# Optimization experiments

Measured on AMD Instinct MI355X. Metric: run time of the kernel, lower is better.

Reference implementation:

```python
import jax, jax.numpy as jnp
import numpy as np

A = 256      # alphabet_size
T = 128      # tag_vector_dim
E = 64       # embedding_dim
H = 64       # hidden_dim (encoder)
NL = 3       # num_layers
B = 4096     # batch
L = 32       # lemma length
STEPS = 30   # decode steps
START = 1    # Alphabet.start_integer (external global in source; fixed here)


def _cell(x, h, c, Wih, Whh, bih, bhh):
    # torch LSTM gate order: i, f, g, o
    g = x @ Wih.T + h @ Whh.T + bih + bhh
    i, f, gg, o = jnp.split(g, 4, axis=-1)
    c = jax.nn.sigmoid(f) * c + jax.nn.sigmoid(i) * jnp.tanh(gg)
    h = jax.nn.sigmoid(o) * jnp.tanh(c)
    return h, c


def _run_layer(xs, Wih, Whh, bih, bhh):
    # xs: [L, B, D] -> ys: [L, B, Hout]; zero initial state (torch default)
    Hout = Whh.shape[1]
    h0 = jnp.zeros((xs.shape[1], Hout), xs.dtype)
    def step(carry, x):
        h, c = _cell(x, carry[0], carry[1], Wih, Whh, bih, bhh)
        return (h, c), h
    _, ys = jax.lax.scan(step, (h0, h0), xs)
    return ys


def setup_inputs() -> dict:
    key = jax.random.key(0)
    ks = jax.random.split(key, 24)
    s = 0.05
    inp = {
        'families': jax.random.randint(ks[0], (B,), 0, 10),
        'languages': jax.random.randint(ks[1], (B,), 0, 20),
        'tags': jax.random.uniform(ks[2], (B, T), dtype=jnp.float32),
        'lemmata': jax.random.randint(ks[3], (B, L), 0, A),
        'emb': jax.random.normal(ks[4], (A, E), jnp.float32) * s,
        # encoder lstm1: layer0 in=T+E, layers 1..2 in=H; hidden=H
        'l1_Wih0': jax.random.normal(ks[5], (4 * H, T + E), jnp.float32) * s,
        'l1_Whh0': jax.random.normal(ks[6], (4 * H, H), jnp.float32) * s,
        'l1_bih0': jnp.zeros((4 * H,), jnp.float32),
        'l1_bhh0': jnp.zeros((4 * H,), jnp.float32),
        'l1_Wih': jax.random.normal(ks[7], (NL - 1, 4 * H, H), jnp.float32) * s,
        'l1_Whh': jax.random.normal(ks[8], (NL - 1, 4 * H, H), jnp.float32) * s,
        'l1_bih': jnp.zeros((NL - 1, 4 * H), jnp.float32),
        'l1_bhh': jnp.zeros((NL - 1, 4 * H), jnp.float32),
        # decoder lstm2: layer0 in=T+A, layers 1..2 in=A; hidden=A
        'l2_Wih0': jax.random.normal(ks[9], (4 * A, T + A), jnp.float32) * s,
        'l2_Whh0': jax.random.normal(ks[10], (4 * A, A), jnp.float32) * s,
        'l2_bih0': jnp.zeros((4 * A,), jnp.float32),
        'l2_bhh0': jnp.zeros((4 * A,), jnp.float32),
        'l2_Wih': jax.random.normal(ks[11], (NL - 1, 4 * A, A), jnp.float32) * s,
        'l2_Whh': jax.random.normal(ks[12], (NL - 1, 4 * A, A), jnp.float32) * s,
        'l2_bih': jnp.zeros((NL - 1, 4 * A), jnp.float32),
        'l2_bhh': jnp.zeros((NL - 1, 4 * A), jnp.float32),
        'lin_W': jax.random.normal(ks[13], (A, A), jnp.float32) * s,
        'lin_b': jnp.zeros((A,), jnp.float32),
    }
    return inp


def reference(families, languages, tags, lemmata, emb,
              l1_Wih0, l1_Whh0, l1_bih0, l1_bhh0, l1_Wih, l1_Whh, l1_bih, l1_bhh,
              l2_Wih0, l2_Whh0, l2_bih0, l2_bhh0, l2_Wih, l2_Whh, l2_bih, l2_bhh,
              lin_W, lin_b):
    tags = tags.astype(jnp.float32)
    # ---- encoder (computed as in source; its output is discarded there too) ----
    x = emb[lemmata]                                   # [B, L, E]
    tags_rep = jnp.broadcast_to(tags[:, None, :], (B, L, T))
    enc_in = jnp.concatenate([x, tags_rep], axis=-1)   # [B, L, E+T]
    ys = jnp.swapaxes(enc_in, 0, 1)                    # [L, B, E+T]
    ys = _run_layer(ys, l1_Wih0, l1_Whh0, l1_bih0, l1_bhh0)
    for k in range(NL - 1):
        ys = _run_layer(ys, l1_Wih[k], l1_Whh[k], l1_bih[k], l1_bhh[k])
    code = ys  # unused downstream, matching original (hidden/cell reset to zero)

    start = jax.nn.one_hot(jnp.full((B,), START), A, dtype=jnp.float32)  # [B, A]
    h0 = jnp.zeros((NL, B, A), jnp.float32)
    c0 = jnp.zeros((NL, B, A), jnp.float32)

    def dstep(carry, _):
        prob, h, c = carry
        xin = jnp.concatenate([prob, tags], axis=-1)   # [B, A+T]
        h0_, c0_ = _cell(xin, h[0], c[0], l2_Wih0, l2_Whh0, l2_bih0, l2_bhh0)
        h1_, c1_ = _cell(h0_, h[1], c[1], l2_Wih[0], l2_Whh[0], l2_bih[0], l2_bhh[0])
        h2_, c2_ = _cell(h1_, h[2], c[2], l2_Wih[1], l2_Whh[1], l2_bih[1], l2_bhh[1])
        pred = jax.nn.sigmoid(h2_ @ lin_W.T + lin_b)   # [B, A]
        new_carry = (pred, jnp.stack([h0_, h1_, h2_]), jnp.stack([c0_, c1_, c2_]))
        return new_carry, (pred, jnp.argmax(pred, axis=-1))

    _, (preds, outs) = jax.lax.scan(dstep, (start, h0, c0), None, length=STEPS)
    probabilities = jnp.concatenate(
        [start[:, None, :], jnp.swapaxes(preds, 0, 1)], axis=1)  # [B, 31, A]
    outputs = jnp.swapaxes(outs, 0, 1)                           # [B, 30]
    return probabilities, outputs
```

## Files before the change

kernel.cpp:

```cpp
#include <hip/hip_runtime.h>
#include <math.h>


typedef float v4 __attribute__((ext_vector_type(4)));

constexpr int Bsz   = 4096;
constexpr int AA    = 256;
constexpr int STEPS = 30;
constexpr int LDP   = 31 * AA;
constexpr long long PROB_N = (long long)Bsz * 31 * AA;

constexpr int WP0_Q = 160 * 1024;
constexpr int WP1_Q = 128 * 1024;
constexpr int WP2_Q = 128 * 1024;
constexpr int WPL_Q = 64 * 256;
constexpr int WP1_BASE = WP0_Q;
constexpr int WP2_BASE = WP1_BASE + WP1_Q;
constexpr int WPL_BASE = WP2_BASE + WP2_Q;
constexpr int WP_TOTAL = WPL_BASE + WPL_Q;

constexpr int XROWS = 1152;

__device__ __forceinline__ float sigf(float x) { return 1.0f / (1.0f + expf(-x)); }

__global__ void repack_kernel(const float* __restrict__ Wih0, const float* __restrict__ Whh0,
                              const float* __restrict__ Wih12, const float* __restrict__ Whh12,
                              const float* __restrict__ linW, float* __restrict__ ws)
{
    int t = blockIdx.x * 256 + threadIdx.x;
    v4 val;
    if (t < WP1_BASE) {
        int cg = t & 15, j = (t >> 4) & 3, c = (t >> 6) & 15, q = t >> 10;
        int grow = j * 256 + c * 16 + cg;
        int k4 = q * 4;
        const float* src = (k4 < 384) ? (Wih0 + grow * 384 + k4)
                                      : (Whh0 + grow * 256 + (k4 - 384));
        val = *reinterpret_cast<const v4*>(src);
    } else if (t < WP2_BASE) {
        int tt = t - WP1_BASE;
        int cg = tt & 15, j = (tt >> 4) & 3, c = (tt >> 6) & 15, q = tt >> 10;
        int grow = j * 256 + c * 16 + cg;
        int k4 = q * 4;
        const float* src = (k4 < 256) ? (Wih12 + grow * 256 + k4)
                                      : (Whh12 + grow * 256 + (k4 - 256));
        val = *reinterpret_cast<const v4*>(src);
    } else if (t < WPL_BASE) {
        int tt = t - WP2_BASE;
        int cg = tt & 15, j = (tt >> 4) & 3, c = (tt >> 6) & 15, q = tt >> 10;
        int grow = j * 256 + c * 16 + cg;
        int k4 = q * 4;
        const float* src = (k4 < 256) ? (Wih12 + 262144 + grow * 256 + k4)
                                      : (Whh12 + 262144 + grow * 256 + (k4 - 256));
        val = *reinterpret_cast<const v4*>(src);
    } else {
        int tt = t - WPL_BASE;
        int cg = tt & 15, c = (tt >> 4) & 15, q = tt >> 8;
        int n = c * 16 + cg;
        val = *reinterpret_cast<const v4*>(linW + n * 256 + q * 4);
    }
    reinterpret_cast<v4*>(ws)[t] = val;
}

#define FMA_BLOCK(W, Xv)                                   \
    _Pragma("unroll")                                      \
    for (int k = 0; k < 4; k++)                            \
        _Pragma("unroll")                                  \
        for (int j = 0; j < 4; j++)                        \
            _Pragma("unroll")                              \
            for (int r = 0; r < 4; r++)                    \
                acc[j][r] += W[j][k] * Xv[k][r];

template<int Q>
__device__ __forceinline__ void lstm_phase(
    const v4* __restrict__ wq, const float* __restrict__ xb,
    const float* __restrict__ bihL, const float* __restrict__ bhhL,
    int u, int rg, float (&cr)[4], float* __restrict__ dst)
{
    float bs[4];
    #pragma unroll
    for (int j = 0; j < 4; j++) bs[j] = bihL[j * 256 + u] + bhhL[j * 256 + u];

    float acc[4][4];
    #pragma unroll
    for (int j = 0; j < 4; j++)
        #pragma unroll
        for (int r = 0; r < 4; r++) acc[j][r] = 0.0f;

    const v4* xq = reinterpret_cast<const v4*>(xb) + rg;
    const v4* wp = wq;
    v4 wa[4], wb[4], xa[4], xc[4];

    #pragma unroll
    for (int j = 0; j < 4; j++) wa[j] = wp[j * 16];
    wp += 1024;
    #pragma unroll
    for (int k = 0; k < 4; k++) xa[k] = xq[k * 4];

    #pragma unroll 1
    for (int q = 0; q < Q - 2; q += 2) {
        #pragma unroll
        for (int j = 0; j < 4; j++) wb[j] = wp[j * 16];
        wp += 1024;
        #pragma unroll
        for (int k = 0; k < 4; k++) xc[k] = xq[(q + 1) * 16 + k * 4];
        FMA_BLOCK(wa, xa)
        #pragma unroll
        for (int j = 0; j < 4; j++) wa[j] = wp[j * 16];
        wp += 1024;
        #pragma unroll
        for (int k = 0; k < 4; k++) xa[k] = xq[(q + 2) * 16 + k * 4];
        FMA_BLOCK(wb, xc)
    }
    #pragma unroll
    for (int j = 0; j < 4; j++) wb[j] = wp[j * 16];
    #pragma unroll
    for (int k = 0; k < 4; k++) xc[k] = xq[(Q - 1) * 16 + k * 4];
    FMA_BLOCK(wa, xa)
    FMA_BLOCK(wb, xc)

    __syncthreads();
    v4 hv;
    #pragma unroll
    for (int r = 0; r < 4; r++) {
        float gi = acc[0][r] + bs[0];
        float gf = acc[1][r] + bs[1];
        float gg = acc[2][r] + bs[2];
        float go = acc[3][r] + bs[3];
        float cn = sigf(gf) * cr[r] + sigf(gi) * tanhf(gg);
        cr[r] = cn;
        hv[r] = sigf(go) * tanhf(cn);
    }
    *reinterpret_cast<v4*>(dst + u * 16 + rg * 4) = hv;
    __syncthreads();
}

__device__ __forceinline__ void lin_phase(
    const v4* __restrict__ wq, const float* __restrict__ xb,
    const float* __restrict__ linb,
    int n, int rg, int m0, int t,
    float* __restrict__ probdst, float* __restrict__ out)
{
    float b = linb[n];
    float acc[4] = {0.f, 0.f, 0.f, 0.f};
    const v4* xq = reinterpret_cast<const v4*>(xb) + rg;
    const v4* wp = wq;
    v4 wa, wb, xa[4], xc[4];

    wa = wp[0]; wp += 256;
    #pragma unroll
    for (int k = 0; k < 4; k++) xa[k] = xq[k * 4];

    #pragma unroll 1
    for (int q = 0; q < 62; q += 2) {
        wb = wp[0]; wp += 256;
        #pragma unroll
        for (int k = 0; k < 4; k++) xc[k] = xq[(q + 1) * 16 + k * 4];
        #pragma unroll
        for (int k = 0; k < 4; k++)
            #pragma unroll
            for (int r = 0; r < 4; r++) acc[r] += wa[k] * xa[k][r];
        wa = wp[0]; wp += 256;
        #pragma unroll
        for (int k = 0; k < 4; k++) xa[k] = xq[(q + 2) * 16 + k * 4];
        #pragma unroll
        for (int k = 0; k < 4; k++)
            #pragma unroll
            for (int r = 0; r < 4; r++) acc[r] += wb[k] * xc[k][r];
    }
    wb = wp[0];
    #pragma unroll
    for (int k = 0; k < 4; k++) xc[k] = xq[63 * 16 + k * 4];
    #pragma unroll
    for (int k = 0; k < 4; k++)
        #pragma unroll
        for (int r = 0; r < 4; r++) acc[r] += wa[k] * xa[k][r];
    #pragma unroll
    for (int k = 0; k < 4; k++)
        #pragma unroll
        for (int r = 0; r < 4; r++) acc[r] += wb[k] * xc[k][r];

    __syncthreads();
    v4 pv;
    #pragma unroll
    for (int r = 0; r < 4; r++) pv[r] = sigf(acc[r] + b);
    *reinterpret_cast<v4*>(probdst + n * 16 + rg * 4) = pv;
    #pragma unroll
    for (int r = 0; r < 4; r++)
        out[(long long)(m0 + rg * 4 + r) * LDP + (long long)(t + 1) * AA + n] = pv[r];
    __syncthreads();
}

__global__ __launch_bounds__(1024, 4) void decode_kernel(
    const float* __restrict__ tags,
    const float* __restrict__ bih0, const float* __restrict__ bhh0,
    const float* __restrict__ bih12, const float* __restrict__ bhh12,
    const float* __restrict__ linb,
    const float* __restrict__ ws,
    float* __restrict__ out)
{
    __shared__ float X[XROWS * 16];
    __shared__ float redv[1024];
    __shared__ int   redi[1024];

    const int tid  = threadIdx.x;
    const int c    = tid >> 6;
    const int lane = tid & 63;
    const int cg   = lane & 15;
    const int rg   = lane >> 4;
    const int u    = c * 16 + cg;
    const int m0   = blockIdx.x * 16;

    for (int i = tid; i < XROWS * 16; i += 1024) X[i] = 0.0f;
    __syncthreads();
    for (int i = tid; i < 128 * 16; i += 1024) {
        int m = i & 15, k = i >> 4;
        X[(256 + k) * 16 + m] = tags[(long long)(m0 + m) * 128 + k];
    }
    if (tid < 16) X[1 * 16 + tid] = 1.0f;
    for (int i = tid; i < 256 * 16; i += 1024) {
        int m = i >> 8, col = i & 255;
        out[(long long)(m0 + m) * LDP + col] = (col == 1) ? 1.0f : 0.0f;
    }
    __syncthreads();

    float cr0[4], cr1[4], cr2[4];
    #pragma unroll
    for (int r = 0; r < 4; r++) { cr0[r] = 0.f; cr1[r] = 0.f; cr2[r] = 0.f; }

    const v4* wsq = reinterpret_cast<const v4*>(ws);
    const v4* w0 = wsq + 0        + c * 64 + cg;
    const v4* w1 = wsq + WP1_BASE + c * 64 + cg;
    const v4* w2 = wsq + WP2_BASE + c * 64 + cg;
    const v4* wl = wsq + WPL_BASE + c * 16 + cg;

    float* hx0 = X + 384 * 16;
    float* hx1 = X + 640 * 16;
    float* hx2 = X + 896 * 16;

    const int arow = tid & 15, sb = tid >> 4;
    float* outputs = out + PROB_N;

    #pragma unroll 1
    for (int t = 0; t < STEPS; t++) {
        lstm_phase<160>(w0, X,   bih0,         bhh0,         u, rg, cr0, hx0);
        lstm_phase<128>(w1, hx0, bih12,        bhh12,        u, rg, cr1, hx1);
        lstm_phase<128>(w2, hx1, bih12 + 1024, bhh12 + 1024, u, rg, cr2, hx2);
        lin_phase(wl, hx2, linb, u, rg, m0, t, X, out);

        float bv = -1.0f; int bi = 0;
        #pragma unroll
        for (int i = 0; i < 4; i++) {
            int uu = sb * 4 + i;
            float v = X[uu * 16 + arow];
            if (v > bv) { bv = v; bi = uu; }
        }
        redv[sb * 16 + arow] = bv;
        redi[sb * 16 + arow] = bi;
        __syncthreads();
        if (tid < 16) {
            float v0 = redv[tid]; int i0 = redi[tid];
            #pragma unroll 1
            for (int s = 1; s < 64; s++) {
                float v = redv[s * 16 + tid]; int ii = redi[s * 16 + tid];
                if (v > v0 || (v == v0 && ii < i0)) { v0 = v; i0 = ii; }
            }
            outputs[(long long)(m0 + tid) * STEPS + t] = (float)i0;
        }
    }
}

extern "C" void kernel_launch(void* const* d_in, const int* in_sizes, int n_in,
                              void* d_out, int out_size, void* d_ws, size_t ws_size,
                              hipStream_t stream) {
    const float* tags  = (const float*)d_in[2];
    const float* Wih0  = (const float*)d_in[13];
    const float* Whh0  = (const float*)d_in[14];
    const float* bih0  = (const float*)d_in[15];
    const float* bhh0  = (const float*)d_in[16];
    const float* Wih12 = (const float*)d_in[17];
    const float* Whh12 = (const float*)d_in[18];
    const float* bih12 = (const float*)d_in[19];
    const float* bhh12 = (const float*)d_in[20];
    const float* linW  = (const float*)d_in[21];
    const float* linb  = (const float*)d_in[22];

    float* out = (float*)d_out;
    float* ws  = (float*)d_ws;

    repack_kernel<<<WP_TOTAL / 256, 256, 0, stream>>>(Wih0, Whh0, Wih12, Whh12,
                                                      linW, ws);
    decode_kernel<<<Bsz / 16, 1024, 0, stream>>>(
        tags, bih0, bhh0, bih12, bhh12, linb, ws, out);
}
```

Measured before the change: 7.847 ms.

## Stream decoder weights into an LDS ring via async global-to-LDS loads

```diff
diff --git a/kernel.cpp b/kernel.cpp
--- a/kernel.cpp
+++ b/kernel.cpp
@@ -22,6 +22,15 @@
 constexpr int XROWS = 1152;
 
 __device__ __forceinline__ float sigf(float x) { return 1.0f / (1.0f + expf(-x)); }
+
+__device__ __forceinline__ void gld16(const float* g, float* l) {
+    __builtin_amdgcn_global_load_lds(
+        (const __attribute__((address_space(1))) float*)g,
+        (__attribute__((address_space(3))) float*)l,
+        16, 0, 0);
+}
+
+#define WAITVM(n) asm volatile("s_waitcnt vmcnt(" #n ")" ::: "memory")
 
 __global__ void repack_kernel(const float* __restrict__ Wih0, const float* __restrict__ Whh0,
                               const float* __restrict__ Wih12, const float* __restrict__ Whh12,
@@ -61,20 +70,38 @@
     reinterpret_cast<v4*>(ws)[t] = val;
 }
 
-#define FMA_BLOCK(W, Xv)                                   \
-    _Pragma("unroll")                                      \
-    for (int k = 0; k < 4; k++)                            \
-        _Pragma("unroll")                                  \
-        for (int j = 0; j < 4; j++)                        \
-            _Pragma("unroll")                              \
-            for (int r = 0; r < 4; r++)                    \
-                acc[j][r] += W[j][k] * Xv[k][r];
+#define LSTM_CHUNK(q)                                                          \
+    {                                                                          \
+        const v4* wv_ = (const v4*)(wbuf + (((q) & 3) << 12)) + cg;            \
+        v4 w_[4], x_[4];                                                       \
+        _Pragma("unroll") for (int j = 0; j < 4; j++) w_[j] = wv_[j * 16];     \
+        _Pragma("unroll") for (int k = 0; k < 4; k++) x_[k] = xq[(q) * 16 + k * 4]; \
+        _Pragma("unroll") for (int k = 0; k < 4; k++)                          \
+            _Pragma("unroll") for (int j = 0; j < 4; j++)                      \
+                _Pragma("unroll") for (int r = 0; r < 4; r++)                  \
+                    acc[j][r] += w_[j][k] * x_[k][r];                          \
+    }
+
+#define LIN_GROUP(g)                                                           \
+    {                                                                          \
+        const v4* wv_ = (const v4*)(wbuf + (((g) & 3) << 12)) + cg;            \
+        _Pragma("unroll") for (int s = 0; s < 4; s++) {                        \
+            v4 w_ = wv_[s * 16];                                               \
+            v4 x_[4];                                                          \
+            _Pragma("unroll") for (int k = 0; k < 4; k++)                      \
+                x_[k] = xq[((g) * 4 + s) * 16 + k * 4];                        \
+            _Pragma("unroll") for (int k = 0; k < 4; k++)                      \
+                _Pragma("unroll") for (int r = 0; r < 4; r++)                  \
+                    acc[r] += w_[k] * x_[k][r];                                \
+        }                                                                      \
+    }
 
 template<int Q>
-__device__ __forceinline__ void lstm_phase(
-    const v4* __restrict__ wq, const float* __restrict__ xb,
+__device__ __forceinline__ void lstm_phase_async(
+    const float* __restrict__ wg, float* __restrict__ wbuf,
+    const float* __restrict__ xb,
     const float* __restrict__ bihL, const float* __restrict__ bhhL,
-    int u, int rg, float (&cr)[4], float* __restrict__ dst)
+    int u, int rg, int cg, float (&cr)[4], float* __restrict__ dst)
 {
     float bs[4];
     #pragma unroll
@@ -87,36 +114,20 @@
         for (int r = 0; r < 4; r++) acc[j][r] = 0.0f;
 
     const v4* xq = reinterpret_cast<const v4*>(xb) + rg;
-    const v4* wp = wq;
-    v4 wa[4], wb[4], xa[4], xc[4];
-
-    #pragma unroll
-    for (int j = 0; j < 4; j++) wa[j] = wp[j * 16];
-    wp += 1024;
-    #pragma unroll
-    for (int k = 0; k < 4; k++) xa[k] = xq[k * 4];
+
+    gld16(wg,            wbuf);
+    gld16(wg +  1 * 4096, wbuf + 1 * 4096);
+    gld16(wg +  2 * 4096, wbuf + 2 * 4096);
 
     #pragma unroll 1
-    for (int q = 0; q < Q - 2; q += 2) {
-        #pragma unroll
-        for (int j = 0; j < 4; j++) wb[j] = wp[j * 16];
-        wp += 1024;
-        #pragma unroll
-        for (int k = 0; k < 4; k++) xc[k] = xq[(q + 1) * 16 + k * 4];
-        FMA_BLOCK(wa, xa)
-        #pragma unroll
-        for (int j = 0; j < 4; j++) wa[j] = wp[j * 16];
-        wp += 1024;
-        #pragma unroll
-        for (int k = 0; k < 4; k++) xa[k] = xq[(q + 2) * 16 + k * 4];
-        FMA_BLOCK(wb, xc)
-    }
-    #pragma unroll
-    for (int j = 0; j < 4; j++) wb[j] = wp[j * 16];
-    #pragma unroll
-    for (int k = 0; k < 4; k++) xc[k] = xq[(Q - 1) * 16 + k * 4];
-    FMA_BLOCK(wa, xa)
-    FMA_BLOCK(wb, xc)
+    for (int q = 0; q < Q - 3; q++) {
+        gld16(wg + (q + 3) * 4096, wbuf + (((q + 3) & 3) << 12));
+        WAITVM(3);
+        LSTM_CHUNK(q)
+    }
+    WAITVM(2); LSTM_CHUNK(Q - 3)
+    WAITVM(1); LSTM_CHUNK(Q - 2)
+    WAITVM(0); LSTM_CHUNK(Q - 1)
 
     __syncthreads();
     v4 hv;
@@ -134,50 +145,29 @@
     __syncthreads();
 }
 
-__device__ __forceinline__ void lin_phase(
-    const v4* __restrict__ wq, const float* __restrict__ xb,
-    const float* __restrict__ linb,
-    int n, int rg, int m0, int t,
+__device__ __forceinline__ void lin_phase_async(
+    const float* __restrict__ wg, float* __restrict__ wbuf,
+    const float* __restrict__ xb, const float* __restrict__ linb,
+    int n, int rg, int cg, int m0, int t,
     float* __restrict__ probdst, float* __restrict__ out)
 {
     float b = linb[n];
     float acc[4] = {0.f, 0.f, 0.f, 0.f};
     const v4* xq = reinterpret_cast<const v4*>(xb) + rg;
-    const v4* wp = wq;
-    v4 wa, wb, xa[4], xc[4];
-
-    wa = wp[0]; wp += 256;
-    #pragma unroll
-    for (int k = 0; k < 4; k++) xa[k] = xq[k * 4];
+
+    gld16(wg,            wbuf);
+    gld16(wg + 1 * 4096, wbuf + 1 * 4096);
+    gld16(wg + 2 * 4096, wbuf + 2 * 4096);
 
     #pragma unroll 1
-    for (int q = 0; q < 62; q += 2) {
-        wb = wp[0]; wp += 256;
-        #pragma unroll
-        for (int k = 0; k < 4; k++) xc[k] = xq[(q + 1) * 16 + k * 4];
-        #pragma unroll
-        for (int k = 0; k < 4; k++)
-            #pragma unroll
-            for (int r = 0; r < 4; r++) acc[r] += wa[k] * xa[k][r];
-        wa = wp[0]; wp += 256;
-        #pragma unroll
-        for (int k = 0; k < 4; k++) xa[k] = xq[(q + 2) * 16 + k * 4];
-        #pragma unroll
-        for (int k = 0; k < 4; k++)
-            #pragma unroll
-            for (int r = 0; r < 4; r++) acc[r] += wb[k] * xc[k][r];
-    }
-    wb = wp[0];
-    #pragma unroll
-    for (int k = 0; k < 4; k++) xc[k] = xq[63 * 16 + k * 4];
-    #pragma unroll
-    for (int k = 0; k < 4; k++)
-        #pragma unroll
-        for (int r = 0; r < 4; r++) acc[r] += wa[k] * xa[k][r];
-    #pragma unroll
-    for (int k = 0; k < 4; k++)
-        #pragma unroll
-        for (int r = 0; r < 4; r++) acc[r] += wb[k] * xc[k][r];
+    for (int g = 0; g < 13; g++) {
+        gld16(wg + (g + 3) * 4096, wbuf + (((g + 3) & 3) << 12));
+        WAITVM(3);
+        LIN_GROUP(g)
+    }
+    WAITVM(2); LIN_GROUP(13)
+    WAITVM(1); LIN_GROUP(14)
+    WAITVM(0); LIN_GROUP(15)
 
     __syncthreads();
     v4 pv;
@@ -199,6 +189,7 @@
     float* __restrict__ out)
 {
     __shared__ float X[XROWS * 16];
+    __shared__ float wring[4 * 4096];
     __shared__ float redv[1024];
     __shared__ int   redi[1024];
 
@@ -227,11 +218,11 @@
     #pragma unroll
     for (int r = 0; r < 4; r++) { cr0[r] = 0.f; cr1[r] = 0.f; cr2[r] = 0.f; }
 
-    const v4* wsq = reinterpret_cast<const v4*>(ws);
-    const v4* w0 = wsq + 0        + c * 64 + cg;
-    const v4* w1 = wsq + WP1_BASE + c * 64 + cg;
-    const v4* w2 = wsq + WP2_BASE + c * 64 + cg;
-    const v4* wl = wsq + WPL_BASE + c * 16 + cg;
+    const float* w0g = ws + ((c * 64 + lane) << 2);
+    const float* w1g = ws + 4 * WP1_BASE + ((c * 64 + lane) << 2);
+    const float* w2g = ws + 4 * WP2_BASE + ((c * 64 + lane) << 2);
+    const float* wlg = ws + 4 * WPL_BASE + ((rg * 256 + c * 16 + cg) << 2);
+    float* wbuf = wring + c * 256;
 
     float* hx0 = X + 384 * 16;
     float* hx1 = X + 640 * 16;
@@ -242,10 +233,10 @@
 
     #pragma unroll 1
     for (int t = 0; t < STEPS; t++) {
-        lstm_phase<160>(w0, X,   bih0,         bhh0,         u, rg, cr0, hx0);
-        lstm_phase<128>(w1, hx0, bih12,        bhh12,        u, rg, cr1, hx1);
-        lstm_phase<128>(w2, hx1, bih12 + 1024, bhh12 + 1024, u, rg, cr2, hx2);
-        lin_phase(wl, hx2, linb, u, rg, m0, t, X, out);
+        lstm_phase_async<160>(w0g, wbuf, X,   bih0,         bhh0,         u, rg, cg, cr0, hx0);
+        lstm_phase_async<128>(w1g, wbuf, hx0, bih12,        bhh12,        u, rg, cg, cr1, hx1);
+        lstm_phase_async<128>(w2g, wbuf, hx1, bih12 + 1024, bhh12 + 1024, u, rg, cg, cr2, hx2);
+        lin_phase_async(wlg, wbuf, hx2, linb, u, rg, cg, m0, t, X, out);
 
         float bv = -1.0f; int bi = 0;
         #pragma unroll
```

New measurement: 7.342 ms. 6.4% less time.
